# Optimization experiments

Hardware: AMD Instinct MI355X
Metric: run time of the kernel (lower is better)

## Reference

```python
import jax, jax.numpy as jnp
import numpy as np

B, S, T, D, H, DF, E = 16, 1024, 512, 512, 8, 2048, 4
DH = D // H
EPS = 1e-5


def setup_inputs() -> dict:
    key = jax.random.key(0)
    ks = iter(jax.random.split(key, 64))

    def nrm(shape, scale=0.02):
        return jax.random.normal(next(ks), shape, dtype=jnp.float32) * scale

    inp = {
        "x": jax.random.normal(next(ks), (B, S, D), dtype=jnp.float32),
        "cross": jax.random.normal(next(ks), (B, T, D), dtype=jnp.float32),
    }
    for p in ("sa", "ca"):
        for w in ("wq", "wk", "wv", "wo"):
            inp[f"{p}_{w}"] = nrm((D, D))
            inp[f"{p}_b{w[1]}"] = jnp.zeros((D,), jnp.float32)
    inp["gate_w"] = nrm((D, E))
    inp["gate_b"] = jnp.zeros((E,), jnp.float32)
    inp["exp_w1"] = nrm((E, D, DF))
    inp["exp_b1"] = jnp.zeros((E, DF), jnp.float32)
    inp["exp_w2"] = nrm((E, DF, D))
    inp["exp_b2"] = jnp.zeros((E, D), jnp.float32)
    for i in (1, 2, 3):
        inp[f"n{i}_g"] = jnp.ones((D,), jnp.float32)
        inp[f"n{i}_b"] = jnp.zeros((D,), jnp.float32)
    return inp


def layer_norm(x, g, b):
    m = x.mean(-1, keepdims=True)
    v = x.var(-1, keepdims=True)
    return (x - m) * jax.lax.rsqrt(v + EPS) * g + b


def mha(q_in, kv_in, wq, bq, wk, bk, wv, bv, wo, bo, causal):
    Bq, Sq, _ = q_in.shape
    Sk = kv_in.shape[1]
    q = (q_in @ wq + bq).reshape(Bq, Sq, H, DH)
    k = (kv_in @ wk + bk).reshape(Bq, Sk, H, DH)
    v = (kv_in @ wv + bv).reshape(Bq, Sk, H, DH)
    scores = jnp.einsum('bshd,bthd->bhst', q, k) / jnp.sqrt(jnp.float32(DH))
    if causal:
        mask = jnp.tril(jnp.ones((Sq, Sk), dtype=bool))
        scores = jnp.where(mask, scores, jnp.float32(-1e9))
    attn = jax.nn.softmax(scores, axis=-1)
    out = jnp.einsum('bhst,bthd->bshd', attn, v).reshape(Bq, Sq, D)
    return out @ wo + bo


def moe_ffn(x, gw, gb, w1, b1, w2, b2):
    gates = jax.nn.softmax(x @ gw + gb, axis=-1)            # [B,S,E]
    h = jax.nn.relu(jnp.einsum('bsd,edf->bsef', x, w1) + b1)  # [B,S,E,DF]
    yo = jnp.einsum('bsef,efd->bsed', h, w2) + b2            # [B,S,E,D]
    y = jnp.einsum('bse,bsed->bsd', gates, yo)
    imp = gates.mean((0, 1))                                 # importance per expert
    aux = jnp.float32(E) * jnp.sum(imp * imp)                # load-balance penalty
    return y, aux


def reference(x, cross,
              sa_wq, sa_bq, sa_wk, sa_bk, sa_wv, sa_bv, sa_wo, sa_bo,
              ca_wq, ca_bq, ca_wk, ca_bk, ca_wv, ca_bv, ca_wo, ca_bo,
              gate_w, gate_b, exp_w1, exp_b1, exp_w2, exp_b2,
              n1_g, n1_b, n2_g, n2_b, n3_g, n3_b):
    # dropout is identity in eval mode
    x = x + mha(x, x, sa_wq, sa_bq, sa_wk, sa_bk, sa_wv, sa_bv, sa_wo, sa_bo, causal=True)
    x = layer_norm(x, n1_g, n1_b)
    x = x + mha(x, cross, ca_wq, ca_bq, ca_wk, ca_bk, ca_wv, ca_bv, ca_wo, ca_bo, causal=False)
    x = layer_norm(x, n2_g, n2_b)
    y, aux_loss = moe_ffn(x, gate_w, gate_b, exp_w1, exp_b1, exp_w2, exp_b2)
    out = layer_norm(x + y, n3_g, n3_b)
    return out, aux_loss
```

## Files before the change

### kernel.cpp

```cpp
#include <hip/hip_runtime.h>
#include <stdint.h>
#include <stddef.h>

typedef unsigned short bf16u;
typedef __attribute__((ext_vector_type(8))) short short8;
typedef __attribute__((ext_vector_type(4))) float f32x4;

__device__ __forceinline__ bf16u f2bf(float f) {
  union { float f; unsigned u; } v; v.f = f;
  unsigned r = v.u + 0x7FFFu + ((v.u >> 16) & 1u);
  return (bf16u)(r >> 16);
}

#define GL16(g, l) __builtin_amdgcn_global_load_lds( \
    (const __attribute__((address_space(1))) unsigned int*)(g), \
    (__attribute__((address_space(3))) unsigned int*)(l), 16, 0, 0)

enum { EPI_BF16 = 0, EPI_RELU_GATE = 1, EPI_QKV = 2, EPI_RES = 3, EPI_F32ACC = 4, EPI_KV = 5 };

template<int EPI>
__global__ __launch_bounds__(256, 2) void gemm_k(
    const bf16u* __restrict__ A, int LDA,
    const bf16u* __restrict__ BT, int LDB,
    const float* __restrict__ bias, const float* __restrict__ res,
    const float* __restrict__ gates,
    bf16u* __restrict__ o1, bf16u* __restrict__ o2, bf16u* __restrict__ o3,
    float* __restrict__ of,
    int N, int K, int slog, int egate0, int firste)
{
  __shared__ bf16u Ab[2][128 * 32];
  __shared__ bf16u Bb[2][128 * 32];
  const int tid = threadIdx.x, lane = tid & 63, w = tid >> 6;
  const int wm = w >> 1, wn = w & 1;
  const int cpx = gridDim.x >> 3;
  const int bid = (blockIdx.x & 7) * cpx + (blockIdx.x >> 3);
  const int nbt = N >> 7;
  const int mt = bid / nbt, nt = bid - mt * nbt;
  const int bm = mt << 7, bn = nt << 7;

  const int srow = lane >> 2;
  const int scol = (lane & 3) << 3;
  const bf16u* ap0 = A + (size_t)(bm + w * 16 + srow) * LDA + scol;
  const bf16u* ap1 = ap0 + (size_t)64 * LDA;
  const bf16u* bp0 = BT + (size_t)(bn + w * 16 + srow) * LDB + scol;
  const bf16u* bp1 = bp0 + (size_t)64 * LDB;

  f32x4 acc[4][4] = {};
  const int NT = K >> 5;

  GL16(ap0, &Ab[0][w * 512]);
  GL16(ap1, &Ab[0][(4 + w) * 512]);
  GL16(bp0, &Bb[0][w * 512]);
  GL16(bp1, &Bb[0][(4 + w) * 512]);
  __syncthreads();

  const int rl = lane & 15, kg = (lane >> 4) << 3;
  int cur = 0;
  for (int kt = 0; kt < NT; ++kt) {
    if (kt + 1 < NT) {
      const int ko = (kt + 1) << 5;
      const int nb = cur ^ 1;
      GL16(ap0 + ko, &Ab[nb][w * 512]);
      GL16(ap1 + ko, &Ab[nb][(4 + w) * 512]);
      GL16(bp0 + ko, &Bb[nb][w * 512]);
      GL16(bp1 + ko, &Bb[nb][(4 + w) * 512]);
    }
    short8 af[4], bfv[4];
    #pragma unroll
    for (int i = 0; i < 4; ++i)
      af[i] = *(const short8*)&Ab[cur][(wm * 64 + i * 16 + rl) * 32 + kg];
    #pragma unroll
    for (int j = 0; j < 4; ++j)
      bfv[j] = *(const short8*)&Bb[cur][(wn * 64 + j * 16 + rl) * 32 + kg];
    #pragma unroll
    for (int i = 0; i < 4; ++i)
      #pragma unroll
      for (int j = 0; j < 4; ++j)
        acc[i][j] = __builtin_amdgcn_mfma_f32_16x16x32_bf16(af[i], bfv[j], acc[i][j], 0, 0, 0);
    __syncthreads();
    cur ^= 1;
  }

  const int r0 = bm + wm * 64, c0 = bn + wn * 64;
  const int rsub = (lane >> 4) << 2;
  #pragma unroll
  for (int j = 0; j < 4; ++j) {
    const int col = c0 + j * 16 + rl;
    const float bs = bias ? bias[col] : 0.f;
    #pragma unroll
    for (int i = 0; i < 4; ++i) {
      const f32x4 v = acc[i][j];
      #pragma unroll
      for (int jj = 0; jj < 4; ++jj) {
        const int row = r0 + i * 16 + rsub + jj;
        const float val = v[jj] + bs;
        if (EPI == EPI_BF16) {
          o1[(size_t)row * N + col] = f2bf(val);
        } else if (EPI == EPI_RELU_GATE) {
          const float g = gates[(size_t)row * 4 + egate0 + (col >> 11)];
          o1[(size_t)row * N + col] = f2bf(g * (val > 0.f ? val : 0.f));
        } else if (EPI == EPI_QKV) {
          if (col < 512) o1[(size_t)row * 512 + col] = f2bf(val);
          else if (col < 1024) o2[(size_t)row * 512 + col - 512] = f2bf(val);
          else {
            const int c = col - 1024;
            const int b_ = row >> slog, t_ = row & ((1 << slog) - 1);
            o3[(((size_t)(b_ * 8 + (c >> 6)) << 6) + (size_t)(c & 63)) * ((size_t)1 << slog) + t_] = f2bf(val);
          }
        } else if (EPI == EPI_KV) {
          if (col < 512) o2[(size_t)row * 512 + col] = f2bf(val);
          else {
            const int c = col - 512;
            const int b_ = row >> slog, t_ = row & ((1 << slog) - 1);
            o3[(((size_t)(b_ * 8 + (c >> 6)) << 6) + (size_t)(c & 63)) * ((size_t)1 << slog) + t_] = f2bf(val);
          }
        } else if (EPI == EPI_RES) {
          of[(size_t)row * N + col] = res[(size_t)row * N + col] + val;
        } else {
          const size_t oi = (size_t)row * N + col;
          of[oi] = firste ? val : (of[oi] + val);
        }
      }
    }
  }
}

template<bool CAUSAL>
__global__ __launch_bounds__(256, 4) void attn_k(
    const bf16u* __restrict__ Q, const bf16u* __restrict__ Kg,
    const bf16u* __restrict__ VT, bf16u* __restrict__ O,
    int Sq, int Sk)
{
  __shared__ bf16u Kl[2][64 * 64];
  __shared__ bf16u Vl[2][64 * 64];
  __shared__ bf16u Pl[64 * 64];
  const int nqt = Sq >> 6;
  const int bh = blockIdx.x / nqt, qt = blockIdx.x - bh * nqt;
  const int b = bh >> 3, h = bh & 7;
  const int tid = threadIdx.x, lane = tid & 63, w = tid >> 6;
  const int rl = lane & 15, g4 = lane >> 4;

  const int qrow = qt * 64 + w * 16 + rl;
  const bf16u* qp = Q + (size_t)(b * Sq + qrow) * 512 + h * 64 + g4 * 8;
  const short8 qf0 = *(const short8*)qp;
  const short8 qf1 = *(const short8*)(qp + 32);

  f32x4 oacc[4] = {};
  float ml = -1e30f, ll = 0.f;
  const int KT = CAUSAL ? (qt + 1) : (Sk >> 6);

  const int str = tid >> 2, stc = tid & 3;
  const int sw_st = (str & 7) << 4;
  const bf16u* kq = Kg + (size_t)(b * Sk + str) * 512 + h * 64 + stc * 8;
  const bf16u* vq = VT + (size_t)(bh * 64 + str) * Sk + stc * 8;
  const int lo0 = str * 128 + ((stc * 16) ^ sw_st);
  const int lo1 = str * 128 + ((stc * 16 + 64) ^ sw_st);

  const int qr = w * 16 + rl;
  char* const pbase = (char*)Pl + qr * 128;
  const int swq = (qr & 7) << 4;

  {
    const short8 k0 = *(const short8*)kq;
    const short8 k1 = *(const short8*)(kq + 32);
    const short8 v0 = *(const short8*)vq;
    const short8 v1 = *(const short8*)(vq + 32);
    *(short8*)((char*)Kl[0] + lo0) = k0;
    *(short8*)((char*)Kl[0] + lo1) = k1;
    *(short8*)((char*)Vl[0] + lo0) = v0;
    *(short8*)((char*)Vl[0] + lo1) = v1;
  }
  __syncthreads();

  int cur = 0;
  for (int kt = 0; kt < KT; ++kt) {
    short8 nk0, nk1, nv0, nv1;
    const bool pre = (kt + 1 < KT);
    if (pre) {
      const bf16u* ks = kq + (size_t)(kt + 1) * 64 * 512;
      const bf16u* vs = vq + (kt + 1) * 64;
      nk0 = *(const short8*)ks;
      nk1 = *(const short8*)(ks + 32);
      nv0 = *(const short8*)vs;
      nv1 = *(const short8*)(vs + 32);
    }

    const bf16u* Kc = Kl[cur];
    const bf16u* Vc = Vl[cur];
    f32x4 st[4] = {};
    #pragma unroll
    for (int mi = 0; mi < 4; ++mi) {
      const int kr = mi * 16 + rl;
      const char* kb_ = (const char*)Kc + kr * 128;
      const int sw = (kr & 7) << 4;
      const short8 kf0 = *(const short8*)(kb_ + ((g4 * 16) ^ sw));
      const short8 kf1 = *(const short8*)(kb_ + ((g4 * 16 + 64) ^ sw));
      st[mi] = __builtin_amdgcn_mfma_f32_16x16x32_bf16(kf0, qf0, st[mi], 0, 0, 0);
      st[mi] = __builtin_amdgcn_mfma_f32_16x16x32_bf16(kf1, qf1, st[mi], 0, 0, 0);
    }

    const float SC = 0.125f * 1.44269504f;
    float sv[16];
    float pm = -1e30f;
    if (CAUSAL && kt == qt) {
      const int qg = qt * 64 + qr;
      #pragma unroll
      for (int mi = 0; mi < 4; ++mi)
        #pragma unroll
        for (int jj = 0; jj < 4; ++jj) {
          float s = st[mi][jj] * SC;
          const int kgi = kt * 64 + mi * 16 + g4 * 4 + jj;
          if (kgi > qg) s = -1e30f;
          sv[mi * 4 + jj] = s;
          pm = fmaxf(pm, s);
        }
    } else {
      #pragma unroll
      for (int mi = 0; mi < 4; ++mi)
        #pragma unroll
        for (int jj = 0; jj < 4; ++jj) {
          const float s = st[mi][jj] * SC;
          sv[mi * 4 + jj] = s;
          pm = fmaxf(pm, s);
        }
    }
    pm = fmaxf(pm, __shfl_xor(pm, 16));
    pm = fmaxf(pm, __shfl_xor(pm, 32));
    const float mnew = fmaxf(ml, pm);
    const float alpha = exp2f(ml - mnew);
    float ps = 0.f;
    bf16u pb[16];
    #pragma unroll
    for (int ii = 0; ii < 16; ++ii) {
      const float p = exp2f(sv[ii] - mnew);
      ps += p;
      pb[ii] = f2bf(p);
    }
    ps += __shfl_xor(ps, 16);
    ps += __shfl_xor(ps, 32);
    ll = ll * alpha + ps;
    ml = mnew;

    #pragma unroll
    for (int jj = 0; jj < 4; ++jj) {
      const float aj = __shfl(alpha, g4 * 4 + jj);
      #pragma unroll
      for (int ni = 0; ni < 4; ++ni) oacc[ni][jj] *= aj;
    }

    #pragma unroll
    for (int mi = 0; mi < 4; ++mi) {
      #pragma unroll
      for (int jp = 0; jp < 2; ++jp) {
        const unsigned pk = (unsigned)pb[mi * 4 + jp * 2] | ((unsigned)pb[mi * 4 + jp * 2 + 1] << 16);
        const int kx2 = mi * 32 + g4 * 8 + jp * 4;
        *(unsigned*)(pbase + (kx2 ^ swq)) = pk;
      }
    }
    asm volatile("s_waitcnt lgkmcnt(0)" ::: "memory");
    #pragma unroll
    for (int ks = 0; ks < 2; ++ks) {
      const short8 pf = *(const short8*)(pbase + ((g4 * 16 + ks * 64) ^ swq));
      #pragma unroll
      for (int ni = 0; ni < 4; ++ni) {
        const int vr = ni * 16 + rl;
        const short8 vf = *(const short8*)((const char*)Vc + vr * 128 + ((g4 * 16 + ks * 64) ^ ((vr & 7) << 4)));
        oacc[ni] = __builtin_amdgcn_mfma_f32_16x16x32_bf16(pf, vf, oacc[ni], 0, 0, 0);
      }
    }

    __syncthreads();
    if (pre) {
      const int nb = cur ^ 1;
      *(short8*)((char*)Kl[nb] + lo0) = nk0;
      *(short8*)((char*)Kl[nb] + lo1) = nk1;
      *(short8*)((char*)Vl[nb] + lo0) = nv0;
      *(short8*)((char*)Vl[nb] + lo1) = nv1;
      __syncthreads();
    }
    cur ^= 1;
  }

  #pragma unroll
  for (int jj = 0; jj < 4; ++jj) {
    const float lj = __shfl(ll, g4 * 4 + jj);
    const float inv = 1.f / lj;
    const int row = qt * 64 + w * 16 + g4 * 4 + jj;
    #pragma unroll
    for (int ni = 0; ni < 4; ++ni)
      O[(size_t)(b * Sq + row) * 512 + h * 64 + ni * 16 + rl] = f2bf(oacc[ni][jj] * inv);
  }
}

template<bool ADD, bool BOUT>
__global__ __launch_bounds__(256, 4) void ln_k(
    const float* __restrict__ X, const float* __restrict__ Y,
    const float* __restrict__ gam, const float* __restrict__ bet,
    float* __restrict__ outf, bf16u* __restrict__ outb)
{
  const int row = blockIdx.x * 4 + (threadIdx.x >> 6);
  const int lane = threadIdx.x & 63;
  const float* xp = X + (size_t)row * 512 + lane * 8;
  float v[8];
  {
    const float4 t0 = *(const float4*)xp;
    const float4 t1 = *(const float4*)(xp + 4);
    v[0] = t0.x; v[1] = t0.y; v[2] = t0.z; v[3] = t0.w;
    v[4] = t1.x; v[5] = t1.y; v[6] = t1.z; v[7] = t1.w;
  }
  if (ADD) {
    const float* yp = Y + (size_t)row * 512 + lane * 8;
    const float4 t0 = *(const float4*)yp;
    const float4 t1 = *(const float4*)(yp + 4);
    v[0] += t0.x; v[1] += t0.y; v[2] += t0.z; v[3] += t0.w;
    v[4] += t1.x; v[5] += t1.y; v[6] += t1.z; v[7] += t1.w;
  }
  float s = 0.f, q = 0.f;
  #pragma unroll
  for (int i = 0; i < 8; ++i) { s += v[i]; q += v[i] * v[i]; }
  #pragma unroll
  for (int off = 1; off < 64; off <<= 1) {
    s += __shfl_xor(s, off);
    q += __shfl_xor(q, off);
  }
  const float mean = s * (1.f / 512.f);
  const float var = q * (1.f / 512.f) - mean * mean;
  const float rs = rsqrtf(var + 1e-5f);
  float o[8];
  #pragma unroll
  for (int i = 0; i < 8; ++i) {
    const float g = gam[lane * 8 + i], bb = bet[lane * 8 + i];
    o[i] = (v[i] - mean) * rs * g + bb;
  }
  float* op = outf + (size_t)row * 512 + lane * 8;
  *(float4*)op = make_float4(o[0], o[1], o[2], o[3]);
  *(float4*)(op + 4) = make_float4(o[4], o[5], o[6], o[7]);
  if (BOUT) {
    union { bf16u u[8]; short8 v8; } pk;
    #pragma unroll
    for (int i = 0; i < 8; ++i) pk.u[i] = f2bf(o[i]);
    *(short8*)(outb + (size_t)row * 512 + lane * 8) = pk.v8;
  }
}

__global__ __launch_bounds__(256, 4) void ln_final_k(
    const float* __restrict__ X, const float* __restrict__ Y,
    const float* __restrict__ gates, const float* __restrict__ b2,
    const float* __restrict__ gam, const float* __restrict__ bet,
    float* __restrict__ outf)
{
  const int row = blockIdx.x * 4 + (threadIdx.x >> 6);
  const int lane = threadIdx.x & 63;
  const float4 gv4 = *(const float4*)(gates + (size_t)row * 4);
  float v[8];
  {
    const float* xp = X + (size_t)row * 512 + lane * 8;
    const float* yp = Y + (size_t)row * 512 + lane * 8;
    const float4 t0 = *(const float4*)xp;
    const float4 t1 = *(const float4*)(xp + 4);
    const float4 u0 = *(const float4*)yp;
    const float4 u1 = *(const float4*)(yp + 4);
    v[0] = t0.x + u0.x; v[1] = t0.y + u0.y; v[2] = t0.z + u0.z; v[3] = t0.w + u0.w;
    v[4] = t1.x + u1.x; v[5] = t1.y + u1.y; v[6] = t1.z + u1.z; v[7] = t1.w + u1.w;
  }
  #pragma unroll
  for (int e = 0; e < 4; ++e) {
    const float ge = e == 0 ? gv4.x : e == 1 ? gv4.y : e == 2 ? gv4.z : gv4.w;
    const float4 b0 = *(const float4*)(b2 + e * 512 + lane * 8);
    const float4 b1 = *(const float4*)(b2 + e * 512 + lane * 8 + 4);
    v[0] += ge * b0.x; v[1] += ge * b0.y; v[2] += ge * b0.z; v[3] += ge * b0.w;
    v[4] += ge * b1.x; v[5] += ge * b1.y; v[6] += ge * b1.z; v[7] += ge * b1.w;
  }
  float s = 0.f, q = 0.f;
  #pragma unroll
  for (int i = 0; i < 8; ++i) { s += v[i]; q += v[i] * v[i]; }
  #pragma unroll
  for (int off = 1; off < 64; off <<= 1) {
    s += __shfl_xor(s, off);
    q += __shfl_xor(q, off);
  }
  const float mean = s * (1.f / 512.f);
  const float var = q * (1.f / 512.f) - mean * mean;
  const float rs = rsqrtf(var + 1e-5f);
  float* op = outf + (size_t)row * 512 + lane * 8;
  float o[8];
  #pragma unroll
  for (int i = 0; i < 8; ++i)
    o[i] = (v[i] - mean) * rs * gam[lane * 8 + i] + bet[lane * 8 + i];
  *(float4*)op = make_float4(o[0], o[1], o[2], o[3]);
  *(float4*)(op + 4) = make_float4(o[4], o[5], o[6], o[7]);
}

__global__ __launch_bounds__(256, 4) void gate_k(
    const float* __restrict__ X, const float* __restrict__ gw,
    const float* __restrict__ gb, float* __restrict__ gates,
    float* __restrict__ imp)
{
  __shared__ float sh[4];
  const int tid = threadIdx.x;
  if (tid < 4) sh[tid] = 0.f;
  __syncthreads();
  const int row = blockIdx.x * 4 + (tid >> 6);
  const int lane = tid & 63;
  const float* xr = X + (size_t)row * 512;
  float a0 = 0.f, a1 = 0.f, a2 = 0.f, a3 = 0.f;
  for (int d = lane; d < 512; d += 64) {
    const float xv = xr[d];
    const float4 wv = *(const float4*)(gw + d * 4);
    a0 += xv * wv.x; a1 += xv * wv.y; a2 += xv * wv.z; a3 += xv * wv.w;
  }
  #pragma unroll
  for (int off = 1; off < 64; off <<= 1) {
    a0 += __shfl_xor(a0, off); a1 += __shfl_xor(a1, off);
    a2 += __shfl_xor(a2, off); a3 += __shfl_xor(a3, off);
  }
  if (lane == 0) {
    a0 += gb[0]; a1 += gb[1]; a2 += gb[2]; a3 += gb[3];
    const float m = fmaxf(fmaxf(a0, a1), fmaxf(a2, a3));
    const float e0 = exp2f((a0 - m) * 1.44269504f);
    const float e1 = exp2f((a1 - m) * 1.44269504f);
    const float e2 = exp2f((a2 - m) * 1.44269504f);
    const float e3 = exp2f((a3 - m) * 1.44269504f);
    const float inv = 1.f / (e0 + e1 + e2 + e3);
    float* gr = gates + (size_t)row * 4;
    const float g0 = e0 * inv, g1 = e1 * inv, g2 = e2 * inv, g3 = e3 * inv;
    gr[0] = g0; gr[1] = g1; gr[2] = g2; gr[3] = g3;
    atomicAdd(&sh[0], g0); atomicAdd(&sh[1], g1);
    atomicAdd(&sh[2], g2); atomicAdd(&sh[3], g3);
  }
  __syncthreads();
  if (tid < 4) atomicAdd(&imp[tid], sh[tid]);
}

__global__ void aux_k(const float* __restrict__ imp, float* __restrict__ out) {
  if (threadIdx.x == 0 && blockIdx.x == 0) {
    float s = 0.f;
    #pragma unroll
    for (int e = 0; e < 4; ++e) { const float v = imp[e] * (1.f / 16384.f); s += v * v; }
    out[0] = 4.f * s;
  }
}

__global__ __launch_bounds__(256, 4) void conv_k(const float* __restrict__ in, bf16u* __restrict__ out) {
  const size_t i = ((size_t)blockIdx.x * 256 + threadIdx.x) * 8;
  const float4 a = *(const float4*)(in + i);
  const float4 b = *(const float4*)(in + i + 4);
  union { bf16u u[8]; short8 v; } pk;
  pk.u[0] = f2bf(a.x); pk.u[1] = f2bf(a.y); pk.u[2] = f2bf(a.z); pk.u[3] = f2bf(a.w);
  pk.u[4] = f2bf(b.x); pk.u[5] = f2bf(b.y); pk.u[6] = f2bf(b.z); pk.u[7] = f2bf(b.w);
  *(short8*)(out + i) = pk.v;
}

__global__ __launch_bounds__(256, 4) void trans_k(
    const float* __restrict__ W, bf16u* __restrict__ WT, int K, int N)
{
  __shared__ float t[32][33];
  const int tx = threadIdx.x & 31, ty = threadIdx.x >> 5;
  const int n0 = blockIdx.x * 32, k0 = blockIdx.y * 32;
  #pragma unroll
  for (int i = 0; i < 4; ++i)
    t[ty + i * 8][tx] = W[(size_t)(k0 + ty + i * 8) * N + n0 + tx];
  __syncthreads();
  #pragma unroll
  for (int i = 0; i < 4; ++i)
    WT[(size_t)(n0 + ty + i * 8) * K + k0 + tx] = f2bf(t[tx][ty + i * 8]);
}

extern "C" void kernel_launch(void* const* d_in, const int* in_sizes, int n_in,
                              void* d_out, int out_size, void* d_ws, size_t ws_size,
                              hipStream_t stream)
{
  const int B = 16, S = 1024, T = 512, D = 512, DF = 2048, E = 4;
  const int M = B * S;
  const int Mc = B * T;
  (void)in_sizes; (void)n_in; (void)out_size;

  const float* x      = (const float*)d_in[0];
  const float* cross  = (const float*)d_in[1];
  const float* gate_w = (const float*)d_in[18];
  const float* gate_b = (const float*)d_in[19];
  const float* exp_w1 = (const float*)d_in[20];
  const float* exp_b1 = (const float*)d_in[21];
  const float* exp_w2 = (const float*)d_in[22];
  const float* exp_b2 = (const float*)d_in[23];

  char* p = (char*)d_ws;
  auto alloc = [&](size_t bytes) -> char* {
    char* r = p;
    p += (bytes + 255) & ~(size_t)255;
    return r;
  };
  bf16u* xb    = (bf16u*)alloc((size_t)M * D * 2);
  bf16u* crb   = (bf16u*)alloc((size_t)Mc * D * 2);
  bf16u* wT    = (bf16u*)alloc((size_t)8 * D * D * 2);
  bf16u* w1T   = (bf16u*)alloc((size_t)E * DF * D * 2);
  bf16u* w2T   = (bf16u*)alloc((size_t)D * E * DF * 2);
  bf16u* qb    = (bf16u*)alloc((size_t)M * D * 2);
  bf16u* kb    = (bf16u*)alloc((size_t)M * D * 2);
  bf16u* vTb   = (bf16u*)alloc((size_t)M * D * 2);
  bf16u* ao    = (bf16u*)alloc((size_t)M * D * 2);
  float* xf    = (float*)alloc((size_t)M * D * 4);
  bf16u* x2b   = (bf16u*)alloc((size_t)M * D * 2);
  float* gates = (float*)alloc((size_t)M * 4 * 4);
  float* imp   = (float*)alloc(256);
  float* y     = (float*)alloc((size_t)M * D * 4);
  float* qkvb  = (float*)alloc(1536 * 4);
  float* kvb   = (float*)alloc(1024 * 4);

  const size_t used = (size_t)(p - (char*)d_ws);
  const size_t perE = (size_t)M * DF * 2;
  const size_t rem = ws_size > used ? ws_size - used : 0;
  const int EC = rem >= 4 * perE + 4096 ? 4 : rem >= 2 * perE + 4096 ? 2 : 1;
  bf16u* hbuf = (bf16u*)alloc((size_t)EC * perE);

  hipMemsetAsync(imp, 0, 32, stream);
  hipMemcpyAsync(qkvb,        d_in[3], 512 * 4, hipMemcpyDeviceToDevice, stream);
  hipMemcpyAsync(qkvb + 512,  d_in[5], 512 * 4, hipMemcpyDeviceToDevice, stream);
  hipMemcpyAsync(qkvb + 1024, d_in[7], 512 * 4, hipMemcpyDeviceToDevice, stream);
  hipMemcpyAsync(kvb,         d_in[13], 512 * 4, hipMemcpyDeviceToDevice, stream);
  hipMemcpyAsync(kvb + 512,   d_in[15], 512 * 4, hipMemcpyDeviceToDevice, stream);

  conv_k<<<(M * D) / 2048, 256, 0, stream>>>(x, xb);
  conv_k<<<(Mc * D) / 2048, 256, 0, stream>>>(cross, crb);
  for (int i = 0; i < 8; ++i)
    trans_k<<<dim3(D / 32, D / 32), 256, 0, stream>>>((const float*)d_in[2 + 2 * i], wT + (size_t)i * D * D, D, D);
  for (int e = 0; e < E; ++e)
    trans_k<<<dim3(DF / 32, D / 32), 256, 0, stream>>>(exp_w1 + (size_t)e * D * DF, w1T + (size_t)e * DF * D, D, DF);
  trans_k<<<dim3(D / 32, (E * DF) / 32), 256, 0, stream>>>(exp_w2, w2T, E * DF, D);

  const int gATT = B * 8 * (S / 64);

  gemm_k<EPI_QKV><<<(M / 128) * 12, 256, 0, stream>>>(
      xb, 512, wT, 512, qkvb, nullptr, nullptr, qb, kb, vTb, nullptr, 1536, 512, 10, 0, 0);
  attn_k<true><<<gATT, 256, 0, stream>>>(qb, kb, vTb, ao, S, S);
  gemm_k<EPI_RES><<<(M / 128) * 4, 256, 0, stream>>>(
      ao, 512, wT + 3 * (size_t)D * D, 512, (const float*)d_in[9], x, nullptr,
      nullptr, nullptr, nullptr, xf, 512, 512, 0, 0, 0);
  ln_k<false, true><<<M / 4, 256, 0, stream>>>(xf, nullptr, (const float*)d_in[24], (const float*)d_in[25], xf, x2b);

  gemm_k<EPI_BF16><<<(M / 128) * 4, 256, 0, stream>>>(
      x2b, 512, wT + 4 * (size_t)D * D, 512, (const float*)d_in[11], nullptr, nullptr,
      qb, nullptr, nullptr, nullptr, 512, 512, 0, 0, 0);
  gemm_k<EPI_KV><<<(Mc / 128) * 8, 256, 0, stream>>>(
      crb, 512, wT + 5 * (size_t)D * D, 512, kvb, nullptr, nullptr,
      nullptr, kb, vTb, nullptr, 1024, 512, 9, 0, 0);
  attn_k<false><<<gATT, 256, 0, stream>>>(qb, kb, vTb, ao, S, T);
  gemm_k<EPI_RES><<<(M / 128) * 4, 256, 0, stream>>>(
      ao, 512, wT + 7 * (size_t)D * D, 512, (const float*)d_in[17], xf, nullptr,
      nullptr, nullptr, nullptr, xf, 512, 512, 0, 0, 0);
  ln_k<false, true><<<M / 4, 256, 0, stream>>>(xf, nullptr, (const float*)d_in[26], (const float*)d_in[27], xf, x2b);

  gate_k<<<M / 4, 256, 0, stream>>>(xf, gate_w, gate_b, gates, imp);
  aux_k<<<1, 64, 0, stream>>>(imp, (float*)d_out + (size_t)M * D);
  const int NC = E / EC;
  const int Nh = EC * DF;
  for (int c = 0; c < NC; ++c) {
    gemm_k<EPI_RELU_GATE><<<(M / 128) * (Nh / 128), 256, 0, stream>>>(
        x2b, 512, w1T + (size_t)c * Nh * D, 512, exp_b1 + (size_t)c * Nh, nullptr, gates,
        hbuf, nullptr, nullptr, nullptr, Nh, 512, 0, c * EC, 0);
    gemm_k<EPI_F32ACC><<<(M / 128) * 4, 256, 0, stream>>>(
        hbuf, Nh, w2T + (size_t)c * Nh, E * DF, nullptr, nullptr, nullptr,
        nullptr, nullptr, nullptr, y, 512, Nh, 0, 0, c == 0 ? 1 : 0);
  }
  ln_final_k<<<M / 4, 256, 0, stream>>>(xf, y, gates, exp_b2, (const float*)d_in[28], (const float*)d_in[29], (float*)d_out);
}
```

Measured before the change: 962.3 us.

## Raise GEMM occupancy, reorder causal attention blocks, alias workspace for experts

Raises the GEMM launch-bounds minimum from two to three blocks per CU. Remaps attention block IDs into an XCD-aware order and schedules causal tiles heaviest-first. Drops one barrier in the attention prefetch loop. Overlays the attention-phase buffers with the expert hidden buffer so more experts can be processed per chunk. The higher occupancy target may force register spills, and the buffer aliasing depends on the attention buffers being dead before the MoE phase.

Result: faster. 893.6 us (-7.1%).

```diff
diff --git a/kernel.cpp b/kernel.cpp
--- a/kernel.cpp
+++ b/kernel.cpp
@@ -19,7 +19,7 @@
 enum { EPI_BF16 = 0, EPI_RELU_GATE = 1, EPI_QKV = 2, EPI_RES = 3, EPI_F32ACC = 4, EPI_KV = 5 };
 
 template<int EPI>
-__global__ __launch_bounds__(256, 2) void gemm_k(
+__global__ __launch_bounds__(256, 3) void gemm_k(
     const bf16u* __restrict__ A, int LDA,
     const bf16u* __restrict__ BT, int LDB,
     const float* __restrict__ bias, const float* __restrict__ res,
@@ -135,7 +135,11 @@
   __shared__ bf16u Vl[2][64 * 64];
   __shared__ bf16u Pl[64 * 64];
   const int nqt = Sq >> 6;
-  const int bh = blockIdx.x / nqt, qt = blockIdx.x - bh * nqt;
+  const int cpx = gridDim.x >> 3;
+  const int bid = (blockIdx.x & 7) * cpx + (blockIdx.x >> 3);
+  const int bh = bid / nqt;
+  int qt = bid - bh * nqt;
+  if (CAUSAL) qt = nqt - 1 - qt;
   const int b = bh >> 3, h = bh & 7;
   const int tid = threadIdx.x, lane = tid & 63, w = tid >> 6;
   const int rl = lane & 15, g4 = lane >> 4;
@@ -269,15 +273,14 @@
       }
     }
 
-    __syncthreads();
     if (pre) {
       const int nb = cur ^ 1;
       *(short8*)((char*)Kl[nb] + lo0) = nk0;
       *(short8*)((char*)Kl[nb] + lo1) = nk1;
       *(short8*)((char*)Vl[nb] + lo0) = nv0;
       *(short8*)((char*)Vl[nb] + lo1) = nv1;
-      __syncthreads();
-    }
+    }
+    __syncthreads();
     cur ^= 1;
   }
 
@@ -490,15 +493,8 @@
     p += (bytes + 255) & ~(size_t)255;
     return r;
   };
-  bf16u* xb    = (bf16u*)alloc((size_t)M * D * 2);
-  bf16u* crb   = (bf16u*)alloc((size_t)Mc * D * 2);
-  bf16u* wT    = (bf16u*)alloc((size_t)8 * D * D * 2);
   bf16u* w1T   = (bf16u*)alloc((size_t)E * DF * D * 2);
   bf16u* w2T   = (bf16u*)alloc((size_t)D * E * DF * 2);
-  bf16u* qb    = (bf16u*)alloc((size_t)M * D * 2);
-  bf16u* kb    = (bf16u*)alloc((size_t)M * D * 2);
-  bf16u* vTb   = (bf16u*)alloc((size_t)M * D * 2);
-  bf16u* ao    = (bf16u*)alloc((size_t)M * D * 2);
   float* xf    = (float*)alloc((size_t)M * D * 4);
   bf16u* x2b   = (bf16u*)alloc((size_t)M * D * 2);
   float* gates = (float*)alloc((size_t)M * 4 * 4);
@@ -507,11 +503,21 @@
   float* qkvb  = (float*)alloc(1536 * 4);
   float* kvb   = (float*)alloc(1024 * 4);
 
-  const size_t used = (size_t)(p - (char*)d_ws);
+  char* upool = p;
+  bf16u* xb  = (bf16u*)upool;
+  bf16u* crb = xb  + (size_t)M * D;
+  bf16u* wT  = crb + (size_t)Mc * D;
+  bf16u* qb  = wT  + (size_t)8 * D * D;
+  bf16u* kb  = qb  + (size_t)M * D;
+  bf16u* vTb = kb  + (size_t)M * D;
+  bf16u* ao  = vTb + (size_t)M * D;
+  const size_t attnPool = ((size_t)M * D * 5 + (size_t)Mc * D + (size_t)8 * D * D) * 2;
+  bf16u* hbuf = (bf16u*)upool;
+  const size_t persistent = (size_t)(upool - (char*)d_ws);
   const size_t perE = (size_t)M * DF * 2;
-  const size_t rem = ws_size > used ? ws_size - used : 0;
-  const int EC = rem >= 4 * perE + 4096 ? 4 : rem >= 2 * perE + 4096 ? 2 : 1;
-  bf16u* hbuf = (bf16u*)alloc((size_t)EC * perE);
+  const size_t rem = ws_size > persistent ? ws_size - persistent : 0;
+  const int EC = (rem >= 4 * perE && rem >= attnPool) ? 4
+               : (rem >= 2 * perE && rem >= attnPool) ? 2 : 1;
 
   hipMemsetAsync(imp, 0, 32, stream);
   hipMemcpyAsync(qkvb,        d_in[3], 512 * 4, hipMemcpyDeviceToDevice, stream);
```
